# Optimization experiments

Measured on AMD Instinct MI355X. Metric: run time of the kernel, lower is better.

Reference implementation:

```python
import jax, jax.numpy as jnp
import numpy as np

SEQ, B, IN, H, L = 512, 64, 512, 512, 2


def setup_inputs() -> dict:
    key = jax.random.key(0)
    ks = jax.random.split(key, 9)
    s = 0.02
    x = jax.random.normal(ks[0], (SEQ, B, IN), dtype=jnp.float32)
    # torch Linear stores weight as [out, in]; stack per layer (IN == H so uniform)
    Wjx = jax.random.normal(ks[1], (L, H, IN), dtype=jnp.float32) * s
    bjx = jax.random.normal(ks[2], (L, H), dtype=jnp.float32) * s
    Wjh = jax.random.normal(ks[3], (L, H, H), dtype=jnp.float32) * s
    bjh = jax.random.normal(ks[4], (L, H), dtype=jnp.float32) * s
    Wkx = jax.random.normal(ks[5], (L, H, IN), dtype=jnp.float32) * s
    bkx = jax.random.normal(ks[6], (L, H), dtype=jnp.float32) * s
    Wkh = jax.random.normal(ks[7], (L, H, H), dtype=jnp.float32) * s
    bkh = jax.random.normal(ks[8], (L, H), dtype=jnp.float32) * s
    return {"x": x, "Wjx": Wjx, "bjx": bjx, "Wjh": Wjh, "bjh": bjh,
            "Wkx": Wkx, "bkx": bkx, "Wkh": Wkh, "bkh": bkh}


def reference(x, Wjx, bjx, Wjh, bjh, Wkx, bkx, Wkh, bkh):
    # x: [SEQ, B, IN]. Returns (outputs [SEQ, B, H], hidden [L, B, H]).
    L_, B_ = Wjx.shape[0], x.shape[1]
    h0 = jnp.zeros((L_, B_, Wjh.shape[1]), dtype=x.dtype)

    def step(hidden, xt):
        inp = xt  # [B, IN]
        new_h = []
        for l in range(L_):
            h = hidden[l]
            j = jax.nn.sigmoid(inp @ Wjx[l].T + bjx[l] + h @ Wjh[l].T + bjh[l])
            k = jax.nn.sigmoid(inp @ Wkx[l].T + bkx[l] + h @ Wkh[l].T + bkh[l])
            h = j * (1.0 - h) + (1.0 - k) * h
            new_h.append(h)
            inp = h
        return jnp.stack(new_h), inp

    hidden, outputs = jax.lax.scan(step, h0, x)
    return outputs, hidden
```

## Files before the change

### kernel.cpp

```cpp
#include <hip/hip_runtime.h>
#include <hip/hip_bf16.h>


#define SEQn 512
#define Bn   64
#define Hn   512
#define RING 8

typedef __bf16 bf16x8 __attribute__((ext_vector_type(8)));
typedef float  f32x4  __attribute__((ext_vector_type(4)));
typedef unsigned u32;

__device__ __forceinline__ u32 cload(const u32* p) {
    return __hip_atomic_load(p, __ATOMIC_RELAXED, __HIP_MEMORY_SCOPE_AGENT);
}
__device__ __forceinline__ void cstore(u32* p, u32 v) {
    __hip_atomic_store(p, v, __ATOMIC_RELAXED, __HIP_MEMORY_SCOPE_AGENT);
}
__device__ __forceinline__ unsigned short f2bf(float f) {
    u32 u = __float_as_uint(f);
    u += 0x7FFFu + ((u >> 16) & 1u);
    return (unsigned short)(u >> 16);
}
__device__ __forceinline__ bf16x8 cvt8(const float* p) {
    bf16x8 r;
#pragma unroll
    for (int i = 0; i < 8; ++i) r[i] = (__bf16)p[i];
    return r;
}

__global__ void __launch_bounds__(256, 1)
rnn_persistent(const float* __restrict__ x,
               const float* __restrict__ Wjx, const float* __restrict__ bjx,
               const float* __restrict__ Wjh, const float* __restrict__ bjh,
               const float* __restrict__ Wkx, const float* __restrict__ bkx,
               const float* __restrict__ Wkh, const float* __restrict__ bkh,
               float* __restrict__ out,
               u32* __restrict__ ring0,
               u32* __restrict__ ring1,
               u32* __restrict__ flags)
{
    const int wg    = blockIdx.x;
    const int layer = wg >> 7;
    const int id    = wg & 127;
    const int mg    = id >> 5;
    const int ng    = id & 31;
    const int tid   = threadIdx.x;
    const int wave  = tid >> 6;
    const int lane  = tid & 63;

    const int ucol = ng * 16 + (lane & 15);
    const int koff = (wave & 1) * 256 + ((lane >> 4) << 3);
    const float* wjsrc = ((wave < 2) ? Wjx : Wjh) + (size_t)layer * Hn * Hn + (size_t)ucol * Hn + koff;
    const float* wksrc = ((wave < 2) ? Wkx : Wkh) + (size_t)layer * Hn * Hn + (size_t)ucol * Hn + koff;
    bf16x8 wj[8], wk[8];
#pragma unroll
    for (int kt = 0; kt < 8; ++kt) {
        wj[kt] = cvt8(wjsrc + kt * 32);
        wk[kt] = cvt8(wksrc + kt * 32);
    }

    const int ml = tid >> 4;
    const int nu = tid & 15;
    const int ue = ng * 16 + nu;
    const int be = mg * 16 + ml;
    const float bje = bjx[layer * Hn + ue] + bjh[layer * Hn + ue];
    const float bke = bkx[layer * Hn + ue] + bkh[layer * Hn + ue];

    __shared__ float part[4][2][16][16];
    __shared__ char  xT[16384];
    __shared__ char  hT[16384];

    const int m = mg * 16 + (lane & 15);

    auto compute_global = [&](const float* Abase) {
        f32x4 aj = {0.f, 0.f, 0.f, 0.f}, ak = {0.f, 0.f, 0.f, 0.f};
        const float* arow = Abase + (size_t)m * Hn + koff;
#pragma unroll
        for (int kt = 0; kt < 8; ++kt) {
            bf16x8 af = cvt8(arow + kt * 32);
            aj = __builtin_amdgcn_mfma_f32_16x16x32_bf16(af, wj[kt], aj, 0, 0, 0);
            ak = __builtin_amdgcn_mfma_f32_16x16x32_bf16(af, wk[kt], ak, 0, 0, 0);
        }
#pragma unroll
        for (int r = 0; r < 4; ++r) {
            part[wave][0][((lane >> 4) << 2) + r][lane & 15] = aj[r];
            part[wave][1][((lane >> 4) << 2) + r][lane & 15] = ak[r];
        }
    };
    auto compute_lds = [&](const char* tile) {
        f32x4 aj = {0.f, 0.f, 0.f, 0.f}, ak = {0.f, 0.f, 0.f, 0.f};
        const int r       = lane & 15;
        const int cb      = ((wave & 1) << 8) + ((lane >> 4) << 3);
        const int swz     = (r & 7) << 4;
        const int rowbase = r << 10;
#pragma unroll
        for (int kt = 0; kt < 8; ++kt) {
            const int c = cb + kt * 32;
            bf16x8 af = *(const bf16x8*)(tile + ((rowbase + (c << 1)) ^ swz));
            aj = __builtin_amdgcn_mfma_f32_16x16x32_bf16(af, wj[kt], aj, 0, 0, 0);
            ak = __builtin_amdgcn_mfma_f32_16x16x32_bf16(af, wk[kt], ak, 0, 0, 0);
        }
#pragma unroll
        for (int r2 = 0; r2 < 4; ++r2) {
            part[wave][0][((lane >> 4) << 2) + r2][lane & 15] = aj[r2];
            part[wave][1][((lane >> 4) << 2) + r2][lane & 15] = ak[r2];
        }
    };

    auto stage = [&](const u32* src, char* dstT, int want) {
        u32 v[32];
        const u32 w = (u32)want;
        while (true) {
            bool ok = true;
#pragma unroll
            for (int b = 0; b < 32; ++b) v[b] = cload(src + (b << 8) + tid);
#pragma unroll
            for (int b = 0; b < 32; ++b) ok &= ((v[b] & 0xFFFFu) == w);
            if (__all(ok)) break;
            __builtin_amdgcn_s_sleep(1);
        }
#pragma unroll
        for (int b = 0; b < 32; ++b) {
            const int d = (b << 8) + tid;
            const int r = d >> 9;
            *(unsigned short*)(dstT + ((d << 1) ^ ((r & 7) << 4))) = (unsigned short)(v[b] >> 16);
        }
    };

    float hprev = 0.f;

    for (int t = 0; t < SEQn; ++t) {
        const int slot  = t & (RING - 1);
        const int pslot = (t - 1) & (RING - 1);
        const u32* hsrc = (layer == 0 ? ring0 : ring1)
                          + (size_t)pslot * Bn * Hn + (size_t)mg * 16 * Hn;
        const u32* xsrc = ring0 + (size_t)slot * Bn * Hn + (size_t)mg * 16 * Hn;

        if (layer == 0 && wave < 2)
            compute_global(x + (size_t)t * Bn * Hn);

        if (layer == 0) {
            u32 v[32];
            const u32 w = (u32)t;
            bool fok = (t < RING);
            const int fwant = t - RING + 1;
            while (true) {
                bool ok = true;
                if (!fok) {
                    int fv = (int)cload(flags + (mg << 5) + (lane & 31));
                    fok = __all(fv >= fwant);
                }
#pragma unroll
                for (int b = 0; b < 32; ++b) v[b] = cload(hsrc + (b << 8) + tid);
#pragma unroll
                for (int b = 0; b < 32; ++b) ok &= ((v[b] & 0xFFFFu) == w);
                if (fok && __all(ok)) break;
                __builtin_amdgcn_s_sleep(1);
            }
#pragma unroll
            for (int b = 0; b < 32; ++b) {
                const int d = (b << 8) + tid;
                const int r = d >> 9;
                *(unsigned short*)(hT + ((d << 1) ^ ((r & 7) << 4))) = (unsigned short)(v[b] >> 16);
            }
        } else {
            stage(hsrc, hT, t);
            stage(xsrc, xT, t + 1);
        }
        __syncthreads();

        if (layer == 1 && tid == 0)
            cstore(flags + (mg << 5) + ng, (u32)(t + 1));

        if (layer == 0) { if (wave >= 2) compute_lds(hT); }
        else            { if (wave < 2) compute_lds(xT); else compute_lds(hT); }
        __syncthreads();

        float sj = part[0][0][ml][nu] + part[1][0][ml][nu] +
                   part[2][0][ml][nu] + part[3][0][ml][nu] + bje;
        float sk = part[0][1][ml][nu] + part[1][1][ml][nu] +
                   part[2][1][ml][nu] + part[3][1][ml][nu] + bke;
        float jj = 1.f / (1.f + __expf(-sj));
        float kk = 1.f / (1.f + __expf(-sk));
        float hnew = jj * (1.f - hprev) + (1.f - kk) * hprev;
        hprev = hnew;

        u32 word = ((u32)f2bf(hnew) << 16) | (u32)(t + 1);
        cstore((layer == 0 ? ring0 : ring1) + (size_t)slot * Bn * Hn + (size_t)be * Hn + ue, word);

        if (layer == 1)
            out[(size_t)t * Bn * Hn + (size_t)be * Hn + ue] = hnew;
        if (t == SEQn - 1)
            out[(size_t)SEQn * Bn * Hn + (size_t)layer * Bn * Hn + (size_t)be * Hn + ue] = hnew;

        __syncthreads();
    }
}

extern "C" void kernel_launch(void* const* d_in, const int* in_sizes, int n_in,
                              void* d_out, int out_size, void* d_ws, size_t ws_size,
                              hipStream_t stream) {
    (void)in_sizes; (void)n_in; (void)out_size; (void)ws_size;

    const float* x   = (const float*)d_in[0];
    const float* Wjx = (const float*)d_in[1];
    const float* bjx = (const float*)d_in[2];
    const float* Wjh = (const float*)d_in[3];
    const float* bjh = (const float*)d_in[4];
    const float* Wkx = (const float*)d_in[5];
    const float* bkx = (const float*)d_in[6];
    const float* Wkh = (const float*)d_in[7];
    const float* bkh = (const float*)d_in[8];
    float* out = (float*)d_out;

    char* ws = (char*)d_ws;
    u32* ring0 = (u32*)ws;
    u32* ring1 = (u32*)(ws + 1048576);
    u32* flags = (u32*)(ws + 2097152);

    hipMemsetAsync(ws, 0, 2097152 + 4096, stream);

    void* args[] = { (void*)&x, (void*)&Wjx, (void*)&bjx, (void*)&Wjh, (void*)&bjh,
                     (void*)&Wkx, (void*)&bkx, (void*)&Wkh, (void*)&bkh,
                     (void*)&out, (void*)&ring0, (void*)&ring1, (void*)&flags };
    hipLaunchCooperativeKernel((void*)rnn_persistent, dim3(256), dim3(256),
                               args, 0, stream);
}
```

Baseline: 2.763 ms.

## Double-buffer partial sums, drop trailing barrier, add sentinel polling and t=0 skip

Double-buffers the LDS partial-sum array by timestep parity, which lets the third __syncthreads per step be removed. Polling first spins on a single sentinel word per row before the full 32-word staging load, which cuts global load traffic while waiting. At t=0 layer 0 skips the recurrent matmul because h is zero. Spin loops get iteration caps as a deadlock guard, and there is a non-cooperative launch fallback. The caps risk reading stale data if a wait ever times out.

```diff
diff --git a/kernel.cpp b/kernel.cpp
--- a/kernel.cpp
+++ b/kernel.cpp
@@ -6,10 +6,15 @@
 #define Bn   64
 #define Hn   512
 #define RING 8
+#define BH   32768
+#define TILE 8192
+
+#define SPIN_MAIN 65536u
 
 typedef __bf16 bf16x8 __attribute__((ext_vector_type(8)));
 typedef float  f32x4  __attribute__((ext_vector_type(4)));
 typedef unsigned u32;
+typedef unsigned long long u64;
 
 __device__ __forceinline__ u32 cload(const u32* p) {
     return __hip_atomic_load(p, __ATOMIC_RELAXED, __HIP_MEMORY_SCOPE_AGENT);
@@ -67,13 +72,13 @@
     const float bje = bjx[layer * Hn + ue] + bjh[layer * Hn + ue];
     const float bke = bkx[layer * Hn + ue] + bkh[layer * Hn + ue];
 
-    __shared__ float part[4][2][16][16];
+    __shared__ float part[2][4][2][16][16];
     __shared__ char  xT[16384];
     __shared__ char  hT[16384];
 
     const int m = mg * 16 + (lane & 15);
 
-    auto compute_global = [&](const float* Abase) {
+    auto compute_global = [&](const float* Abase, int pb) {
         f32x4 aj = {0.f, 0.f, 0.f, 0.f}, ak = {0.f, 0.f, 0.f, 0.f};
         const float* arow = Abase + (size_t)m * Hn + koff;
 #pragma unroll
@@ -84,11 +89,11 @@
         }
 #pragma unroll
         for (int r = 0; r < 4; ++r) {
-            part[wave][0][((lane >> 4) << 2) + r][lane & 15] = aj[r];
-            part[wave][1][((lane >> 4) << 2) + r][lane & 15] = ak[r];
-        }
-    };
-    auto compute_lds = [&](const char* tile) {
+            part[pb][wave][0][((lane >> 4) << 2) + r][lane & 15] = aj[r];
+            part[pb][wave][1][((lane >> 4) << 2) + r][lane & 15] = ak[r];
+        }
+    };
+    auto compute_lds = [&](const char* tile, int pb) {
         f32x4 aj = {0.f, 0.f, 0.f, 0.f}, ak = {0.f, 0.f, 0.f, 0.f};
         const int r       = lane & 15;
         const int cb      = ((wave & 1) << 8) + ((lane >> 4) << 3);
@@ -103,98 +108,103 @@
         }
 #pragma unroll
         for (int r2 = 0; r2 < 4; ++r2) {
-            part[wave][0][((lane >> 4) << 2) + r2][lane & 15] = aj[r2];
-            part[wave][1][((lane >> 4) << 2) + r2][lane & 15] = ak[r2];
-        }
-    };
-
-    auto stage = [&](const u32* src, char* dstT, int want) {
+            part[pb][wave][0][((lane >> 4) << 2) + r2][lane & 15] = aj[r2];
+            part[pb][wave][1][((lane >> 4) << 2) + r2][lane & 15] = ak[r2];
+        }
+    };
+    auto zero_store = [&](int pb) {
+#pragma unroll
+        for (int r2 = 0; r2 < 4; ++r2) {
+            part[pb][wave][0][((lane >> 4) << 2) + r2][lane & 15] = 0.f;
+            part[pb][wave][1][((lane >> 4) << 2) + r2][lane & 15] = 0.f;
+        }
+    };
+    auto stage_llc = [&](const u32* src, char* dstT, u32 want, bool sent) {
+        if (sent) {
+            const int p = tid & 31;
+            const u32* sp = src + (((p & 15) << 9) | (p << 4) | 15);
+            u32 it = 0;
+            while (true) {
+                u32 s = cload(sp);
+                if (__all((s & 0xFFFFu) == want)) break;
+                if (++it > SPIN_MAIN) break;
+                __builtin_amdgcn_s_sleep(1);
+            }
+        }
         u32 v[32];
-        const u32 w = (u32)want;
+        u32 it = 0;
         while (true) {
             bool ok = true;
 #pragma unroll
             for (int b = 0; b < 32; ++b) v[b] = cload(src + (b << 8) + tid);
 #pragma unroll
-            for (int b = 0; b < 32; ++b) ok &= ((v[b] & 0xFFFFu) == w);
+            for (int b = 0; b < 32; ++b) ok &= ((v[b] & 0xFFFFu) == want);
             if (__all(ok)) break;
+            if (++it > SPIN_MAIN) break;
             __builtin_amdgcn_s_sleep(1);
         }
 #pragma unroll
         for (int b = 0; b < 32; ++b) {
-            const int d = (b << 8) + tid;
-            const int r = d >> 9;
-            *(unsigned short*)(dstT + ((d << 1) ^ ((r & 7) << 4))) = (unsigned short)(v[b] >> 16);
+            const int d = (b << 8) + tid, r = d >> 9;
+            *(unsigned short*)(dstT + ((d << 1) ^ ((r & 7) << 4))) =
+                (unsigned short)(v[b] >> 16);
+        }
+    };
+    auto bpf_wait = [&](int want) {
+        u32 it = 0;
+        while (true) {
+            int fv = (int)cload(flags + (mg << 5) + (lane & 31));
+            if (__all(fv >= want)) break;
+            if (++it > SPIN_MAIN) break;
+            __builtin_amdgcn_s_sleep(1);
         }
     };
 
     float hprev = 0.f;
 
     for (int t = 0; t < SEQn; ++t) {
+        const int pb    = t & 1;
         const int slot  = t & (RING - 1);
         const int pslot = (t - 1) & (RING - 1);
         const u32* hsrc = (layer == 0 ? ring0 : ring1)
-                          + (size_t)pslot * Bn * Hn + (size_t)mg * 16 * Hn;
-        const u32* xsrc = ring0 + (size_t)slot * Bn * Hn + (size_t)mg * 16 * Hn;
+                          + (size_t)pslot * BH + mg * TILE;
+        const u32* xsrc = ring0 + (size_t)slot * BH + mg * TILE;
 
         if (layer == 0 && wave < 2)
-            compute_global(x + (size_t)t * Bn * Hn);
+            compute_global(x + (size_t)t * BH, pb);
 
         if (layer == 0) {
-            u32 v[32];
-            const u32 w = (u32)t;
-            bool fok = (t < RING);
-            const int fwant = t - RING + 1;
-            while (true) {
-                bool ok = true;
-                if (!fok) {
-                    int fv = (int)cload(flags + (mg << 5) + (lane & 31));
-                    fok = __all(fv >= fwant);
-                }
-#pragma unroll
-                for (int b = 0; b < 32; ++b) v[b] = cload(hsrc + (b << 8) + tid);
-#pragma unroll
-                for (int b = 0; b < 32; ++b) ok &= ((v[b] & 0xFFFFu) == w);
-                if (fok && __all(ok)) break;
-                __builtin_amdgcn_s_sleep(1);
-            }
-#pragma unroll
-            for (int b = 0; b < 32; ++b) {
-                const int d = (b << 8) + tid;
-                const int r = d >> 9;
-                *(unsigned short*)(hT + ((d << 1) ^ ((r & 7) << 4))) = (unsigned short)(v[b] >> 16);
-            }
+            if (t >= RING) bpf_wait(t - RING + 1);
+            if (t > 0) stage_llc(hsrc, hT, (u32)t, true);
         } else {
-            stage(hsrc, hT, t);
-            stage(xsrc, xT, t + 1);
+            stage_llc(hsrc, hT, (u32)t, false);
+            stage_llc(xsrc, xT, (u32)(t + 1), true);
         }
         __syncthreads();
 
         if (layer == 1 && tid == 0)
             cstore(flags + (mg << 5) + ng, (u32)(t + 1));
 
-        if (layer == 0) { if (wave >= 2) compute_lds(hT); }
-        else            { if (wave < 2) compute_lds(xT); else compute_lds(hT); }
+        if (layer == 0) { if (wave >= 2) { if (t > 0) compute_lds(hT, pb); else zero_store(pb); } }
+        else            { if (wave < 2) compute_lds(xT, pb); else compute_lds(hT, pb); }
         __syncthreads();
 
-        float sj = part[0][0][ml][nu] + part[1][0][ml][nu] +
-                   part[2][0][ml][nu] + part[3][0][ml][nu] + bje;
-        float sk = part[0][1][ml][nu] + part[1][1][ml][nu] +
-                   part[2][1][ml][nu] + part[3][1][ml][nu] + bke;
+        float sj = part[pb][0][0][ml][nu] + part[pb][1][0][ml][nu] +
+                   part[pb][2][0][ml][nu] + part[pb][3][0][ml][nu] + bje;
+        float sk = part[pb][0][1][ml][nu] + part[pb][1][1][ml][nu] +
+                   part[pb][2][1][ml][nu] + part[pb][3][1][ml][nu] + bke;
         float jj = 1.f / (1.f + __expf(-sj));
         float kk = 1.f / (1.f + __expf(-sk));
         float hnew = jj * (1.f - hprev) + (1.f - kk) * hprev;
         hprev = hnew;
 
         u32 word = ((u32)f2bf(hnew) << 16) | (u32)(t + 1);
-        cstore((layer == 0 ? ring0 : ring1) + (size_t)slot * Bn * Hn + (size_t)be * Hn + ue, word);
+        cstore((layer == 0 ? ring0 : ring1) + (size_t)slot * BH + (size_t)be * Hn + ue, word);
 
         if (layer == 1)
-            out[(size_t)t * Bn * Hn + (size_t)be * Hn + ue] = hnew;
+            out[(size_t)t * BH + (size_t)be * Hn + ue] = hnew;
         if (t == SEQn - 1)
-            out[(size_t)SEQn * Bn * Hn + (size_t)layer * Bn * Hn + (size_t)be * Hn + ue] = hnew;
-
-        __syncthreads();
+            out[(size_t)SEQn * BH + (size_t)layer * BH + (size_t)be * Hn + ue] = hnew;
     }
 }
 
@@ -224,6 +234,11 @@
     void* args[] = { (void*)&x, (void*)&Wjx, (void*)&bjx, (void*)&Wjh, (void*)&bjh,
                      (void*)&Wkx, (void*)&bkx, (void*)&Wkh, (void*)&bkh,
                      (void*)&out, (void*)&ring0, (void*)&ring1, (void*)&flags };
-    hipLaunchCooperativeKernel((void*)rnn_persistent, dim3(256), dim3(256),
-                               args, 0, stream);
-}
+    hipError_t err = hipLaunchCooperativeKernel((void*)rnn_persistent, dim3(256),
+                                                dim3(256), args, 0, stream);
+    if (err != hipSuccess) {
+        hipLaunchKernelGGL(rnn_persistent, dim3(256), dim3(256), 0, stream,
+                           x, Wjx, bjx, Wjh, bjh, Wkx, bkx, Wkh, bkh,
+                           out, ring0, ring1, flags);
+    }
+}
```

Result: faster. 2.691 ms (-2.6%).
